# Kernel optimization log

Measured on AMD Instinct MI355X. Metric: run time of the kernel, lower is better.

Reference implementation:

```python
import jax, jax.numpy as jnp
import numpy as np

# ---- static configuration (matches init_kwargs / input_specs) ----
B, N = 4, 128            # images, proposals per image
C = 256                  # feature channels (in_channels)
HF, WF = 23, 30          # feature map size (input 736x960 / 32)
PH, PW = 7, 7            # pooled_size
SCALE = 1.0 / 32.0       # scale_factor
HIMG, WIMG = HF * 32, WF * 32
KH = HF // PH + 2        # max rows any pooling bin can span
KW = WF // PW + 2        # max cols any pooling bin can span
HID, OUT = 256, 5
NEG = -1e30


def _roi_pool_one(f, box):
    """Quantized ROI max pooling for one proposal.
    f: (C, HF, WF) feature map; box: (4,) [x1,y1,x2,y2] in feature coords.
    Returns (C, PH, PW)."""
    box = jax.lax.stop_gradient(box)  # indices are non-differentiable
    x1 = jnp.clip(jnp.floor(box[0]).astype(jnp.int32), 0, WF - 1)
    y1 = jnp.clip(jnp.floor(box[1]).astype(jnp.int32), 0, HF - 1)
    roi_w = jnp.clip(jnp.ceil(box[2]).astype(jnp.int32) - x1, 1, WF)
    roi_h = jnp.clip(jnp.ceil(box[3]).astype(jnp.int32) - y1, 1, HF)
    ph = jnp.arange(PH)
    pw = jnp.arange(PW)
    hs = y1 + (ph * roi_h) // PH                       # bin row starts (PH,)
    he = y1 + ((ph + 1) * roi_h + PH - 1) // PH        # bin row ends (ceil)
    ws = x1 + (pw * roi_w) // PW
    we = x1 + ((pw + 1) * roi_w + PW - 1) // PW
    hidx = hs[:, None] + jnp.arange(KH)[None, :]       # (PH, KH)
    hval = (hidx < he[:, None]) & (hidx < HF)
    widx = ws[:, None] + jnp.arange(KW)[None, :]       # (PW, KW)
    wval = (widx < we[:, None]) & (widx < WF)
    rows = f[:, jnp.clip(hidx, 0, HF - 1), :]          # (C, PH, KH, WF) gather
    rmax = jnp.max(jnp.where(hval[None, :, :, None], rows, NEG), axis=2)  # (C, PH, WF)
    cols = rmax[:, :, jnp.clip(widx, 0, WF - 1)]       # (C, PH, PW, KW) gather
    return jnp.max(jnp.where(wval[None, None], cols, NEG), axis=3)        # (C, PH, PW)


# vmap over proposals, then over images: (B,C,HF,WF),(B,N,4) -> (B,N,C,PH,PW)
_roi_pool = jax.vmap(jax.vmap(_roi_pool_one, in_axes=(None, 0)), in_axes=(0, 0))


def setup_inputs() -> dict:
    key = jax.random.key(0)
    ks = jax.random.split(key, 8)
    features = jax.random.normal(ks[0], (B, C, HF, WF), jnp.float32)
    # valid proposals in image coordinates (min box side ~32 px)
    x1 = jax.random.uniform(ks[1], (B, N)) * (WIMG - 32.0)
    y1 = jax.random.uniform(ks[2], (B, N)) * (HIMG - 32.0)
    x2 = x1 + 32.0 + jax.random.uniform(ks[3], (B, N)) * (WIMG - 32.0 - x1)
    y2 = y1 + 32.0 + jax.random.uniform(ks[4], (B, N)) * (HIMG - 32.0 - y1)
    conf = jax.random.normal(ks[5], (B, N))
    proposals = jnp.stack([x1, y1, x2, y2, conf], axis=-1)  # (B, N, 5)
    W1 = jax.random.normal(ks[6], (HID, C * PH * PW), jnp.float32) * 0.01
    b1 = jnp.zeros((HID,), jnp.float32)
    W2 = jax.random.normal(ks[7], (OUT, HID), jnp.float32) * 0.01
    b2 = jnp.zeros((OUT,), jnp.float32)
    return {"features": features, "proposals": proposals,
            "W1": W1, "b1": b1, "W2": W2, "b2": b2}


def reference(features, proposals, W1, b1, W2, b2):
    boxes_feat = proposals[..., :4] * SCALE                 # image -> feature coords
    pooled = _roi_pool(features, boxes_feat)                # (B, N, C, PH, PW)
    flat = pooled.reshape(B, N, C * PH * PW)
    h = jax.nn.relu(jnp.einsum('bnf,hf->bnh', flat, W1) + b1)
    out = jnp.einsum('bnh,oh->bno', h, W2) + b2             # (B, N, 5)
    refined_boxes = proposals[..., :4] + out[..., :4]
    refined_conf = jax.nn.sigmoid(proposals[..., 4:5] + out[..., 4:5])
    return jnp.concatenate([refined_boxes, refined_conf], axis=-1)  # (B, N, 5)
```

## Files before the change

kernel.cpp:

```cpp
#include <hip/hip_runtime.h>
#include <math.h>

#define Bq 4
#define Nq 128
#define Cq 256
#define HFq 23
#define WFq 30
#define PHq 7
#define PWq 7
#define HIDq 256
#define OUTq 5
#define Fq (Cq*PHq*PWq)
#define Mq (Bq*Nq)
#define HWq (HFq*WFq)
#define SCALEq (1.0f/32.0f)
#define NEGq (-1e30f)
#define KHq 5
#define KWq 6
#define SPLITK 8
#define KCH (Fq/SPLITK)
#define KSTEPS (KCH/32)
#define TJOBS 704

typedef float f32x4 __attribute__((ext_vector_type(4)));
typedef __bf16 bf16x8 __attribute__((ext_vector_type(8)));

__device__ __forceinline__ unsigned short f2b(float f) {
    unsigned int u = __float_as_uint(f);
    unsigned int r = (u + 0x7FFFu + ((u >> 16) & 1u)) >> 16;
    return (unsigned short)r;
}
__device__ __forceinline__ float b2f(unsigned short s) {
    return __uint_as_float(((unsigned int)s) << 16);
}

union PrepSM {
    float t[32][33];
    unsigned short s[Fq];
};

__global__ __launch_bounds__(256) void k_prep(const float* __restrict__ feat,
                                              const float* __restrict__ W1,
                                              unsigned short* __restrict__ ft,
                                              unsigned short* __restrict__ w1p) {
    __shared__ __align__(16) PrepSM sm;
    int tid = threadIdx.x, bid = blockIdx.x;
    if (bid < TJOBS) {
        int bb = bid / 176;
        int rem = bid - bb * 176;
        int cblk = rem / 22;
        int xblk = rem - cblk * 22;
        const float* src = feat + (size_t)bb * Cq * HWq;
        unsigned short* dst = ft + (size_t)bb * HWq * Cq;
        int x0 = xblk * 32, c0 = cblk * 32;
        int tx = tid & 31, ty = tid >> 5;
#pragma unroll
        for (int i = 0; i < 4; ++i) {
            int c = c0 + ty + i * 8, x = x0 + tx;
            if (x < HWq) sm.t[ty + i * 8][tx] = src[(size_t)c * HWq + x];
        }
        __syncthreads();
#pragma unroll
        for (int i = 0; i < 4; ++i) {
            int x = x0 + ty + i * 8, c = c0 + tx;
            if (x < HWq) dst[(size_t)x * Cq + c] = f2b(sm.t[tx][ty + i * 8]);
        }
    } else {
        int j = bid - TJOBS;
        const float4* src = (const float4*)(W1 + (size_t)j * Fq);
        for (int i = tid; i < Fq / 4; i += 256) {
            float4 v = src[i];
            ushort4 o;
            o.x = f2b(v.x); o.y = f2b(v.y); o.z = f2b(v.z); o.w = f2b(v.w);
            ((ushort4*)sm.s)[i] = o;
        }
        __syncthreads();
        uint4* dst = (uint4*)(w1p + (size_t)j * Fq);
        for (int i = tid; i < Fq / 8; i += 256) {
            int base = i * 8;
            int cell = base >> 8;
            int c0 = base & 255;
            unsigned short tmp[8];
#pragma unroll
            for (int u = 0; u < 8; ++u) tmp[u] = sm.s[(c0 + u) * 49 + cell];
            dst[i] = *(const uint4*)tmp;
        }
    }
}

__global__ __launch_bounds__(256) void k_pool(const unsigned short* __restrict__ ft,
                                              const float* __restrict__ props,
                                              unsigned short* __restrict__ pooled) {
    int wave = threadIdx.x >> 6;
    int lane = threadIdx.x & 63;
    int g = blockIdx.y * 4 + wave;
    int m = blockIdx.x;
    int b = m >> 7;
    const float* pr = props + (size_t)m * 5;
    float b0 = pr[0] * SCALEq, b1v = pr[1] * SCALEq;
    float b2v = pr[2] * SCALEq, b3v = pr[3] * SCALEq;
    int x1 = min(max((int)floorf(b0), 0), WFq - 1);
    int y1 = min(max((int)floorf(b1v), 0), HFq - 1);
    int rw = min(max((int)ceilf(b2v) - x1, 1), WFq);
    int rh = min(max((int)ceilf(b3v) - y1, 1), HFq);
    const unsigned short* ftb = ft + (size_t)b * HWq * Cq + lane * 4;
    unsigned short* pm = pooled + (size_t)m * Fq + lane * 4;

    for (int cell = g; cell < PHq * PWq; cell += 8) {
        int ph = cell / 7;
        int pw = cell - ph * 7;
        int hs = y1 + (ph * rh) / PHq;
        int he = min(y1 + ((ph + 1) * rh + PHq - 1) / PHq, HFq);
        int wss = x1 + (pw * rw) / PWq;
        int wee = min(x1 + ((pw + 1) * rw + PWq - 1) / PWq, WFq);
        f32x4 acc = {NEGq, NEGq, NEGq, NEGq};
#pragma unroll
        for (int kh = 0; kh < KHq; ++kh) {
            if (hs + kh < he) {
                const unsigned short* rowp = ftb + (size_t)((hs + kh) * WFq) * Cq;
#pragma unroll
                for (int kw = 0; kw < KWq; ++kw) {
                    if (wss + kw < wee) {
                        ushort4 v = *(const ushort4*)(rowp + (size_t)(wss + kw) * Cq);
                        acc.x = fmaxf(acc.x, b2f(v.x));
                        acc.y = fmaxf(acc.y, b2f(v.y));
                        acc.z = fmaxf(acc.z, b2f(v.z));
                        acc.w = fmaxf(acc.w, b2f(v.w));
                    }
                }
            }
        }
        ushort4 o;
        o.x = f2b(acc.x); o.y = f2b(acc.y); o.z = f2b(acc.z); o.w = f2b(acc.w);
        *(ushort4*)(pm + (size_t)cell * Cq) = o;
    }
}

__global__ __launch_bounds__(256) void k_gemm1(const unsigned short* __restrict__ pooled,
                                               const unsigned short* __restrict__ w1p,
                                               float* __restrict__ part) {
    __shared__ __align__(16) unsigned short As[2][2048];
    __shared__ __align__(16) unsigned short Bs[2][2048];
    int m0 = blockIdx.x * 64;
    int j0 = blockIdx.y * 64;
    int kz = blockIdx.z;
    int tid = threadIdx.x;
    int r = tid >> 2, qq = tid & 3;
    const uint4* ap = (const uint4*)(pooled + (size_t)(m0 + r) * Fq + (size_t)kz * KCH + qq * 8);
    const uint4* bp = (const uint4*)(w1p + (size_t)(j0 + r) * Fq + (size_t)kz * KCH + qq * 8);
    int lane = tid & 63, wv = tid >> 6;
    int q = lane >> 4, mr = lane & 15;
    f32x4 acc0 = {0.f, 0.f, 0.f, 0.f};
    f32x4 acc1 = {0.f, 0.f, 0.f, 0.f};
    f32x4 acc2 = {0.f, 0.f, 0.f, 0.f};
    f32x4 acc3 = {0.f, 0.f, 0.f, 0.f};
    uint4 av = ap[0];
    uint4 bv = bp[0];
    for (int s = 0; s < KSTEPS; ++s) {
        int p = s & 1;
        *(uint4*)(&As[p][tid * 8]) = av;
        *(uint4*)(&Bs[p][tid * 8]) = bv;
        __syncthreads();
        if (s + 1 < KSTEPS) {
            av = ap[(s + 1) * 4];
            bv = bp[(s + 1) * 4];
        }
        const unsigned short* Ab = As[p];
        const unsigned short* Bb = Bs[p];
        bf16x8 a = *(const bf16x8*)(Ab + (wv * 16 + mr) * 32 + q * 8);
        acc0 = __builtin_amdgcn_mfma_f32_16x16x32_bf16(a, *(const bf16x8*)(Bb + (0  + mr) * 32 + q * 8), acc0, 0, 0, 0);
        acc1 = __builtin_amdgcn_mfma_f32_16x16x32_bf16(a, *(const bf16x8*)(Bb + (16 + mr) * 32 + q * 8), acc1, 0, 0, 0);
        acc2 = __builtin_amdgcn_mfma_f32_16x16x32_bf16(a, *(const bf16x8*)(Bb + (32 + mr) * 32 + q * 8), acc2, 0, 0, 0);
        acc3 = __builtin_amdgcn_mfma_f32_16x16x32_bf16(a, *(const bf16x8*)(Bb + (48 + mr) * 32 + q * 8), acc3, 0, 0, 0);
    }
    float* pbase = part + (size_t)kz * Mq * HIDq;
    int mb = m0 + wv * 16 + q * 4;
    int jj = j0 + mr;
#pragma unroll
    for (int r2 = 0; r2 < 4; ++r2) {
        float* row = pbase + (size_t)(mb + r2) * HIDq + jj;
        row[0]  = acc0[r2];
        row[16] = acc1[r2];
        row[32] = acc2[r2];
        row[48] = acc3[r2];
    }
}

__global__ __launch_bounds__(256) void k_tail(const float* __restrict__ part,
                                              const float* __restrict__ b1,
                                              const float* __restrict__ W2,
                                              const float* __restrict__ b2,
                                              const float* __restrict__ props,
                                              float* __restrict__ out) {
    __shared__ float red[OUTq][4];
    int m = blockIdx.x, j = threadIdx.x;
    float s = 0.f;
#pragma unroll
    for (int z = 0; z < SPLITK; ++z) s += part[((size_t)z * Mq + m) * HIDq + j];
    s += b1[j];
    float hv = fmaxf(s, 0.f);
    float p[OUTq];
#pragma unroll
    for (int o = 0; o < OUTq; ++o) p[o] = hv * W2[(size_t)o * HIDq + j];
    int lane = j & 63, wid = j >> 6;
#pragma unroll
    for (int o = 0; o < OUTq; ++o) {
        float v = p[o];
        v += __shfl_xor(v, 1);
        v += __shfl_xor(v, 2);
        v += __shfl_xor(v, 4);
        v += __shfl_xor(v, 8);
        v += __shfl_xor(v, 16);
        v += __shfl_xor(v, 32);
        if (lane == 0) red[o][wid] = v;
    }
    __syncthreads();
    if (j < OUTq) {
        float sv = red[j][0] + red[j][1] + red[j][2] + red[j][3] + b2[j];
        float pv = props[(size_t)m * 5 + j];
        float rr;
        if (j < 4) rr = pv + sv;
        else rr = 1.f / (1.f + expf(-(pv + sv)));
        out[(size_t)m * 5 + j] = rr;
    }
}

extern "C" void kernel_launch(void* const* d_in, const int* in_sizes, int n_in,
                              void* d_out, int out_size, void* d_ws, size_t ws_size,
                              hipStream_t stream) {
    const float* feat  = (const float*)d_in[0];
    const float* props = (const float*)d_in[1];
    const float* W1    = (const float*)d_in[2];
    const float* b1    = (const float*)d_in[3];
    const float* W2    = (const float*)d_in[4];
    const float* b2    = (const float*)d_in[5];
    float* out = (float*)d_out;

    char* ws = (char*)d_ws;
    unsigned short* ft     = (unsigned short*)(ws);
    unsigned short* w1p    = (unsigned short*)(ws + 1413120);
    unsigned short* pooled = (unsigned short*)(ws + 7835648);
    float* part            = (float*)(ws + 20680704);

    k_prep<<<TJOBS + HIDq, 256, 0, stream>>>(feat, W1, ft, w1p);
    k_pool<<<dim3(Mq, 2), 256, 0, stream>>>(ft, props, pooled);
    k_gemm1<<<dim3(8, 4, SPLITK), 256, 0, stream>>>(pooled, w1p, part);
    k_tail<<<Mq, 256, 0, stream>>>(part, b1, W2, b2, props, out);
}
```

Before: 131.2 us.

## Enlarge GEMM tiles to 128x128, raise split-K, store bf16 partials

Measured after the change: 143.3 us. +9.2%, slower.

```diff
diff --git a/kernel.cpp b/kernel.cpp
--- a/kernel.cpp
+++ b/kernel.cpp
@@ -17,9 +17,10 @@
 #define NEGq (-1e30f)
 #define KHq 5
 #define KWq 6
-#define SPLITK 8
+#define SPLITK 56
 #define KCH (Fq/SPLITK)
 #define KSTEPS (KCH/32)
+#define LDP 40
 #define TJOBS 704
 
 typedef float f32x4 __attribute__((ext_vector_type(4)));
@@ -138,55 +139,71 @@
 
 __global__ __launch_bounds__(256) void k_gemm1(const unsigned short* __restrict__ pooled,
                                                const unsigned short* __restrict__ w1p,
-                                               float* __restrict__ part) {
-    __shared__ __align__(16) unsigned short As[2][2048];
-    __shared__ __align__(16) unsigned short Bs[2][2048];
-    int m0 = blockIdx.x * 64;
-    int j0 = blockIdx.y * 64;
+                                               unsigned short* __restrict__ part) {
+    __shared__ __align__(16) unsigned short As[2][128 * LDP];
+    __shared__ __align__(16) unsigned short Bs[2][128 * LDP];
+    int m0 = blockIdx.x * 128;
+    int j0 = blockIdx.y * 128;
     int kz = blockIdx.z;
     int tid = threadIdx.x;
-    int r = tid >> 2, qq = tid & 3;
-    const uint4* ap = (const uint4*)(pooled + (size_t)(m0 + r) * Fq + (size_t)kz * KCH + qq * 8);
-    const uint4* bp = (const uint4*)(w1p + (size_t)(j0 + r) * Fq + (size_t)kz * KCH + qq * 8);
+    int r = tid >> 2, sg = tid & 3;
+    const uint4* apg  = (const uint4*)(pooled + (size_t)(m0 + r) * Fq + kz * KCH + sg * 8);
+    const uint4* apg2 = (const uint4*)(pooled + (size_t)(m0 + r + 64) * Fq + kz * KCH + sg * 8);
+    const uint4* bpg  = (const uint4*)(w1p + (size_t)(j0 + r) * Fq + kz * KCH + sg * 8);
+    const uint4* bpg2 = (const uint4*)(w1p + (size_t)(j0 + r + 64) * Fq + kz * KCH + sg * 8);
+
     int lane = tid & 63, wv = tid >> 6;
     int q = lane >> 4, mr = lane & 15;
-    f32x4 acc0 = {0.f, 0.f, 0.f, 0.f};
-    f32x4 acc1 = {0.f, 0.f, 0.f, 0.f};
-    f32x4 acc2 = {0.f, 0.f, 0.f, 0.f};
-    f32x4 acc3 = {0.f, 0.f, 0.f, 0.f};
-    uint4 av = ap[0];
-    uint4 bv = bp[0];
+    f32x4 acc[2][8];
+#pragma unroll
+    for (int a = 0; a < 2; ++a)
+#pragma unroll
+        for (int b = 0; b < 8; ++b) acc[a][b] = (f32x4){0.f, 0.f, 0.f, 0.f};
+
+    uint4 rA0[2], rA1[2], rB0[2], rB1[2];
+    rA0[0] = apg[0]; rA1[0] = apg2[0]; rB0[0] = bpg[0]; rB1[0] = bpg2[0];
+    rA0[1] = apg[4]; rA1[1] = apg2[4]; rB0[1] = bpg[4]; rB1[1] = bpg2[4];
+
     for (int s = 0; s < KSTEPS; ++s) {
         int p = s & 1;
-        *(uint4*)(&As[p][tid * 8]) = av;
-        *(uint4*)(&Bs[p][tid * 8]) = bv;
+        *(uint4*)(&As[p][r * LDP + sg * 8])        = rA0[p];
+        *(uint4*)(&As[p][(r + 64) * LDP + sg * 8]) = rA1[p];
+        *(uint4*)(&Bs[p][r * LDP + sg * 8])        = rB0[p];
+        *(uint4*)(&Bs[p][(r + 64) * LDP + sg * 8]) = rB1[p];
         __syncthreads();
-        if (s + 1 < KSTEPS) {
-            av = ap[(s + 1) * 4];
-            bv = bp[(s + 1) * 4];
+        if (s + 2 < KSTEPS) {
+            rA0[p] = apg[(s + 2) * 4];
+            rA1[p] = apg2[(s + 2) * 4];
+            rB0[p] = bpg[(s + 2) * 4];
+            rB1[p] = bpg2[(s + 2) * 4];
         }
         const unsigned short* Ab = As[p];
         const unsigned short* Bb = Bs[p];
-        bf16x8 a = *(const bf16x8*)(Ab + (wv * 16 + mr) * 32 + q * 8);
-        acc0 = __builtin_amdgcn_mfma_f32_16x16x32_bf16(a, *(const bf16x8*)(Bb + (0  + mr) * 32 + q * 8), acc0, 0, 0, 0);
-        acc1 = __builtin_amdgcn_mfma_f32_16x16x32_bf16(a, *(const bf16x8*)(Bb + (16 + mr) * 32 + q * 8), acc1, 0, 0, 0);
-        acc2 = __builtin_amdgcn_mfma_f32_16x16x32_bf16(a, *(const bf16x8*)(Bb + (32 + mr) * 32 + q * 8), acc2, 0, 0, 0);
-        acc3 = __builtin_amdgcn_mfma_f32_16x16x32_bf16(a, *(const bf16x8*)(Bb + (48 + mr) * 32 + q * 8), acc3, 0, 0, 0);
-    }
-    float* pbase = part + (size_t)kz * Mq * HIDq;
-    int mb = m0 + wv * 16 + q * 4;
-    int jj = j0 + mr;
-#pragma unroll
-    for (int r2 = 0; r2 < 4; ++r2) {
-        float* row = pbase + (size_t)(mb + r2) * HIDq + jj;
-        row[0]  = acc0[r2];
-        row[16] = acc1[r2];
-        row[32] = acc2[r2];
-        row[48] = acc3[r2];
-    }
-}
-
-__global__ __launch_bounds__(256) void k_tail(const float* __restrict__ part,
+        bf16x8 af0 = *(const bf16x8*)(Ab + (wv * 32 + mr) * LDP + q * 8);
+        bf16x8 af1 = *(const bf16x8*)(Ab + (wv * 32 + 16 + mr) * LDP + q * 8);
+#pragma unroll
+        for (int jf = 0; jf < 8; ++jf) {
+            bf16x8 bf = *(const bf16x8*)(Bb + (jf * 16 + mr) * LDP + q * 8);
+            acc[0][jf] = __builtin_amdgcn_mfma_f32_16x16x32_bf16(af0, bf, acc[0][jf], 0, 0, 0);
+            acc[1][jf] = __builtin_amdgcn_mfma_f32_16x16x32_bf16(af1, bf, acc[1][jf], 0, 0, 0);
+        }
+    }
+    unsigned short* pbase = part + (size_t)kz * Mq * HIDq;
+#pragma unroll
+    for (int mf = 0; mf < 2; ++mf) {
+        int mb = m0 + wv * 32 + mf * 16 + q * 4;
+#pragma unroll
+        for (int jf = 0; jf < 8; ++jf) {
+            int jj = j0 + jf * 16 + mr;
+#pragma unroll
+            for (int r2 = 0; r2 < 4; ++r2) {
+                pbase[(size_t)(mb + r2) * HIDq + jj] = f2b(acc[mf][jf][r2]);
+            }
+        }
+    }
+}
+
+__global__ __launch_bounds__(256) void k_tail(const unsigned short* __restrict__ part,
                                               const float* __restrict__ b1,
                                               const float* __restrict__ W2,
                                               const float* __restrict__ b2,
@@ -196,7 +213,7 @@
     int m = blockIdx.x, j = threadIdx.x;
     float s = 0.f;
 #pragma unroll
-    for (int z = 0; z < SPLITK; ++z) s += part[((size_t)z * Mq + m) * HIDq + j];
+    for (int z = 0; z < SPLITK; ++z) s += b2f(part[((size_t)z * Mq + m) * HIDq + j]);
     s += b1[j];
     float hv = fmaxf(s, 0.f);
     float p[OUTq];
@@ -240,10 +257,10 @@
     unsigned short* ft     = (unsigned short*)(ws);
     unsigned short* w1p    = (unsigned short*)(ws + 1413120);
     unsigned short* pooled = (unsigned short*)(ws + 7835648);
-    float* part            = (float*)(ws + 20680704);
+    unsigned short* part   = (unsigned short*)(ws + 20680704);
 
     k_prep<<<TJOBS + HIDq, 256, 0, stream>>>(feat, W1, ft, w1p);
     k_pool<<<dim3(Mq, 2), 256, 0, stream>>>(ft, props, pooled);
-    k_gemm1<<<dim3(8, 4, SPLITK), 256, 0, stream>>>(pooled, w1p, part);
+    k_gemm1<<<dim3(4, 2, SPLITK), 256, 0, stream>>>(pooled, w1p, part);
     k_tail<<<Mq, 256, 0, stream>>>(part, b1, W2, b2, props, out);
 }
```

## Restructure GEMM1 to register-direct MFMA tiles with wider split-K

Applied to the files above, without the earlier changes.

Result: slower. 134.8 us (+2.7%).

```diff
diff --git a/kernel.cpp b/kernel.cpp
--- a/kernel.cpp
+++ b/kernel.cpp
@@ -17,7 +17,7 @@
 #define NEGq (-1e30f)
 #define KHq 5
 #define KWq 6
-#define SPLITK 8
+#define SPLITK 56
 #define KCH (Fq/SPLITK)
 #define KSTEPS (KCH/32)
 #define TJOBS 704
@@ -139,50 +139,66 @@
 __global__ __launch_bounds__(256) void k_gemm1(const unsigned short* __restrict__ pooled,
                                                const unsigned short* __restrict__ w1p,
                                                float* __restrict__ part) {
-    __shared__ __align__(16) unsigned short As[2][2048];
-    __shared__ __align__(16) unsigned short Bs[2][2048];
+    int tid = threadIdx.x;
+    int wv = tid >> 6, lane = tid & 63;
+    int q = lane >> 4, mr = lane & 15;
     int m0 = blockIdx.x * 64;
-    int j0 = blockIdx.y * 64;
-    int kz = blockIdx.z;
-    int tid = threadIdx.x;
-    int r = tid >> 2, qq = tid & 3;
-    const uint4* ap = (const uint4*)(pooled + (size_t)(m0 + r) * Fq + (size_t)kz * KCH + qq * 8);
-    const uint4* bp = (const uint4*)(w1p + (size_t)(j0 + r) * Fq + (size_t)kz * KCH + qq * 8);
-    int lane = tid & 63, wv = tid >> 6;
-    int q = lane >> 4, mr = lane & 15;
-    f32x4 acc0 = {0.f, 0.f, 0.f, 0.f};
-    f32x4 acc1 = {0.f, 0.f, 0.f, 0.f};
-    f32x4 acc2 = {0.f, 0.f, 0.f, 0.f};
-    f32x4 acc3 = {0.f, 0.f, 0.f, 0.f};
-    uint4 av = ap[0];
-    uint4 bv = bp[0];
+    int j0 = wv * 64;
+    int kz = blockIdx.y;
+
+    const uint4* ap[4];
+    const uint4* bp[4];
+#pragma unroll
+    for (int g = 0; g < 4; ++g) {
+        ap[g] = (const uint4*)(pooled + (size_t)(m0 + g * 16 + mr) * Fq + kz * KCH + q * 8);
+        bp[g] = (const uint4*)(w1p   + (size_t)(j0 + g * 16 + mr) * Fq + kz * KCH + q * 8);
+    }
+
+    f32x4 acc[4][4];
+#pragma unroll
+    for (int a = 0; a < 4; ++a)
+#pragma unroll
+        for (int b = 0; b < 4; ++b) acc[a][b] = (f32x4){0.f, 0.f, 0.f, 0.f};
+
+    uint4 abuf[3][4], bbuf[3][4];
+#pragma unroll
+    for (int g = 0; g < 4; ++g) {
+        abuf[0][g] = ap[g][0]; bbuf[0][g] = bp[g][0];
+        abuf[1][g] = ap[g][4]; bbuf[1][g] = bp[g][4];
+    }
+#pragma unroll
     for (int s = 0; s < KSTEPS; ++s) {
-        int p = s & 1;
-        *(uint4*)(&As[p][tid * 8]) = av;
-        *(uint4*)(&Bs[p][tid * 8]) = bv;
-        __syncthreads();
-        if (s + 1 < KSTEPS) {
-            av = ap[(s + 1) * 4];
-            bv = bp[(s + 1) * 4];
-        }
-        const unsigned short* Ab = As[p];
-        const unsigned short* Bb = Bs[p];
-        bf16x8 a = *(const bf16x8*)(Ab + (wv * 16 + mr) * 32 + q * 8);
-        acc0 = __builtin_amdgcn_mfma_f32_16x16x32_bf16(a, *(const bf16x8*)(Bb + (0  + mr) * 32 + q * 8), acc0, 0, 0, 0);
-        acc1 = __builtin_amdgcn_mfma_f32_16x16x32_bf16(a, *(const bf16x8*)(Bb + (16 + mr) * 32 + q * 8), acc1, 0, 0, 0);
-        acc2 = __builtin_amdgcn_mfma_f32_16x16x32_bf16(a, *(const bf16x8*)(Bb + (32 + mr) * 32 + q * 8), acc2, 0, 0, 0);
-        acc3 = __builtin_amdgcn_mfma_f32_16x16x32_bf16(a, *(const bf16x8*)(Bb + (48 + mr) * 32 + q * 8), acc3, 0, 0, 0);
+        int cur = s % 3;
+        int nxt = (s + 2) % 3;
+        if (s + 2 < KSTEPS) {
+#pragma unroll
+            for (int g = 0; g < 4; ++g) {
+                abuf[nxt][g] = ap[g][(s + 2) * 4];
+                bbuf[nxt][g] = bp[g][(s + 2) * 4];
+            }
+        }
+#pragma unroll
+        for (int mg = 0; mg < 4; ++mg) {
+            bf16x8 af = *(const bf16x8*)&abuf[cur][mg];
+#pragma unroll
+            for (int jg = 0; jg < 4; ++jg) {
+                bf16x8 bf = *(const bf16x8*)&bbuf[cur][jg];
+                acc[mg][jg] = __builtin_amdgcn_mfma_f32_16x16x32_bf16(af, bf, acc[mg][jg], 0, 0, 0);
+            }
+        }
     }
     float* pbase = part + (size_t)kz * Mq * HIDq;
-    int mb = m0 + wv * 16 + q * 4;
-    int jj = j0 + mr;
-#pragma unroll
-    for (int r2 = 0; r2 < 4; ++r2) {
-        float* row = pbase + (size_t)(mb + r2) * HIDq + jj;
-        row[0]  = acc0[r2];
-        row[16] = acc1[r2];
-        row[32] = acc2[r2];
-        row[48] = acc3[r2];
+#pragma unroll
+    for (int mg = 0; mg < 4; ++mg) {
+        int mb = m0 + mg * 16 + q * 4;
+#pragma unroll
+        for (int jg = 0; jg < 4; ++jg) {
+            int jj = j0 + jg * 16 + mr;
+#pragma unroll
+            for (int r2 = 0; r2 < 4; ++r2) {
+                pbase[(size_t)(mb + r2) * HIDq + jj] = acc[mg][jg][r2];
+            }
+        }
     }
 }
 
@@ -244,6 +260,6 @@
 
     k_prep<<<TJOBS + HIDq, 256, 0, stream>>>(feat, W1, ft, w1p);
     k_pool<<<dim3(Mq, 2), 256, 0, stream>>>(ft, props, pooled);
-    k_gemm1<<<dim3(8, 4, SPLITK), 256, 0, stream>>>(pooled, w1p, part);
+    k_gemm1<<<dim3(8, SPLITK), 256, 0, stream>>>(pooled, w1p, part);
     k_tail<<<Mq, 256, 0, stream>>>(part, b1, W2, b2, props, out);
 }
```
